# Optimization experiments

Measured on AMD Instinct MI355X. Metric: run time of the kernel, lower is better.

## Reference

```python
import jax, jax.numpy as jnp
import numpy as np

B, D, H, HD, L = 2, 768, 16, 48, 3
N_IMG, N_PAST, T_DEC = 1024, 16, 20

def _ln(x, g, b, eps=1e-5):
    m = jnp.mean(x, axis=-1, keepdims=True)
    v = jnp.mean(jnp.square(x - m), axis=-1, keepdims=True)
    return (x - m) * jax.lax.rsqrt(v + eps) * g + b

def _encoder(x, ln1_g, ln1_b, qkv_W, qkv_b, out_W, out_b, ln2_g, ln2_b, ff1_W, ff1_b, ff2_W, ff2_b):
    Bs, S, _ = x.shape
    keep = jnp.tril(jnp.ones((S, S), dtype=bool))  # causal: True = attend
    neg = jnp.asarray(jnp.finfo(x.dtype).min, x.dtype)
    scale = 1.0 / np.sqrt(HD)
    for l in range(L):  # pre-norm TransformerEncoderLayer, activation=relu (torch default)
        h = _ln(x, ln1_g[l], ln1_b[l])
        q, k, v = jnp.split(h @ qkv_W[l] + qkv_b[l], 3, axis=-1)
        q = q.reshape(Bs, S, H, HD); k = k.reshape(Bs, S, H, HD); v = v.reshape(Bs, S, H, HD)
        scores = jnp.einsum('bqhd,bkhd->bhqk', q, k) * scale
        attn = jax.nn.softmax(jnp.where(keep, scores, neg), axis=-1)
        ctx = jnp.einsum('bhqk,bkhd->bqhd', attn, v).reshape(Bs, S, H * HD)
        x = x + ctx @ out_W[l] + out_b[l]
        h = _ln(x, ln2_g[l], ln2_b[l])
        x = x + jax.nn.relu(h @ ff1_W[l] + ff1_b[l]) @ ff2_W[l] + ff2_b[l]
    return x

def setup_inputs():
    key = jax.random.key(0)
    ks = jax.random.split(key, 16)
    rn = lambda i, shp, s=0.02: jax.random.normal(ks[i], shp, jnp.float32) * s
    return {
        'feats': jax.random.normal(ks[0], (B, D, N_IMG), jnp.float32),
        'past': jax.random.normal(ks[1], (B, N_PAST, 6), jnp.float32),
        'intent': jax.random.randint(ks[2], (B,), 0, 3),
        'img_pos_enc': rn(3, (1, N_IMG, D)),
        'time_embeds': rn(4, (36, D)),
        'intent_embeds': rn(5, (3, D)),
        'past_W': rn(6, (6, D)), 'past_b': jnp.zeros((D,), jnp.float32),
        'pos_W': rn(7, (2, D)), 'pos_b': jnp.zeros((D,), jnp.float32),
        'ln1_g': jnp.ones((L, D), jnp.float32), 'ln1_b': jnp.zeros((L, D), jnp.float32),
        'qkv_W': rn(8, (L, D, 3 * D)), 'qkv_b': jnp.zeros((L, 3 * D), jnp.float32),
        'out_W': rn(9, (L, D, D)), 'out_b': jnp.zeros((L, D), jnp.float32),
        'ln2_g': jnp.ones((L, D), jnp.float32), 'ln2_b': jnp.zeros((L, D), jnp.float32),
        'ff1_W': rn(10, (L, D, 4 * D)), 'ff1_b': jnp.zeros((L, 4 * D), jnp.float32),
        'ff2_W': rn(11, (L, 4 * D, D)), 'ff2_b': jnp.zeros((L, D), jnp.float32),
        'dec1_W': rn(12, (D, D)), 'dec1_b': jnp.zeros((D,), jnp.float32),
        'dec2_W': rn(13, (D, 2)), 'dec2_b': jnp.zeros((2,), jnp.float32),
    }

def reference(feats, past, intent, img_pos_enc, time_embeds, intent_embeds,
              past_W, past_b, pos_W, pos_b,
              ln1_g, ln1_b, qkv_W, qkv_b, out_W, out_b, ln2_g, ln2_b,
              ff1_W, ff1_b, ff2_W, ff2_b, dec1_W, dec1_b, dec2_W, dec2_b):
    # context: 1024 image tokens + 1 intent token + 16 past tokens
    img_tokens = jnp.transpose(feats, (0, 2, 1)) + img_pos_enc          # [B, 1024, D]
    intent_idx = jnp.clip(intent - 1, 0, 2)
    intent_tok = intent_embeds[intent_idx][:, None, :]                  # [B, 1, D]
    past_toks = past @ past_W + past_b + time_embeds[:N_PAST]           # [B, 16, D]
    seq = jnp.concatenate([img_tokens, intent_tok, past_toks], axis=1)  # [B, 1041, D]
    enc = lambda s: _encoder(s, ln1_g, ln1_b, qkv_W, qkv_b, out_W, out_b,
                             ln2_g, ln2_b, ff1_W, ff1_b, ff2_W, ff2_b)
    preds = []
    for t in range(T_DEC):  # AR decode: full recompute each step, no KV cache (as in source)
        out = enc(seq)
        h = out[:, -1:, :]
        p = jax.nn.gelu(h @ dec1_W + dec1_b, approximate=False) @ dec2_W + dec2_b  # [B,1,2]
        preds.append(p)
        nxt = p @ pos_W + pos_b + time_embeds[N_PAST + t]
        seq = jnp.concatenate([seq, nxt], axis=1)
    return jnp.concatenate(preds, axis=1)  # [B, 20, 2]
```

## Files before the change

### kernel.cpp

```cpp
#include <hip/hip_runtime.h>
#include <math.h>

#define BB 2
#define DD 768
#define HH 16
#define HDIM 48
#define LL 3
#define NIMG 1024
#define NPAST 16
#define TDEC 20
#define SEQ0 1041
#define SPAD 1064
#define MM (BB*SEQ0)
#define SCALE_QK 0.14433756729740643f
#define KVL_C ((size_t)BB*HH*SPAD*HDIM)

typedef __attribute__((ext_vector_type(4))) float f32x4;
typedef __attribute__((ext_vector_type(8))) short bf16x8;

__device__ __forceinline__ short f2bf(float x) {
  unsigned u = __float_as_uint(x);
  unsigned r = (u + 0x7FFFu + ((u >> 16) & 1u)) >> 16;
  return (short)r;
}
__device__ __forceinline__ float bf2f(short h) {
  return __uint_as_float(((unsigned)(unsigned short)h) << 16);
}

__device__ __forceinline__ float block_sum256(float v, float* red) {
#pragma unroll
  for (int off = 32; off; off >>= 1) v += __shfl_down(v, off);
  __syncthreads();
  if ((threadIdx.x & 63) == 0) red[threadIdx.x >> 6] = v;
  __syncthreads();
  return red[0] + red[1] + red[2] + red[3];
}

__global__ __launch_bounds__(256) void build_img_kernel(
    const float* __restrict__ feats, const float* __restrict__ pe, float* __restrict__ x)
{
  __shared__ float T[64][65];
  int b = blockIdx.y;
  int s0 = blockIdx.x * 64;
  int tid = threadIdx.x;
  int r = tid >> 2;
  int c0 = (tid & 3) << 4;
  for (int d0 = 0; d0 < 768; d0 += 64) {
    const float* fp = feats + ((size_t)b*768 + d0 + r)*1024 + s0 + c0;
#pragma unroll
    for (int i = 0; i < 16; ++i) T[r][c0 + i] = fp[i];
    __syncthreads();
    float* xp = x + ((size_t)(b*SEQ0 + s0 + r))*768 + d0 + c0;
    const float* pp = pe + (size_t)(s0 + r)*768 + d0 + c0;
#pragma unroll
    for (int i = 0; i < 16; ++i) xp[i] = T[c0 + i][r] + pp[i];
    __syncthreads();
  }
}

__global__ __launch_bounds__(256) void build_misc_kernel(
    const float* __restrict__ past, const int* __restrict__ intent,
    const float* __restrict__ int_emb, const float* __restrict__ past_W,
    const float* __restrict__ past_b, const float* __restrict__ te,
    float* __restrict__ x)
{
  int b = blockIdx.y;
  int i = blockIdx.x;
  int tid = threadIdx.x;
  if (i == 0) {
    int idx = intent[b] - 1;
    idx = max(0, min(2, idx));
    for (int d = tid; d < 768; d += 256)
      x[((size_t)(b*SEQ0 + 1024))*768 + d] = int_emb[idx*768 + d];
  } else {
    int pi = i - 1;
    float p0 = past[(b*NPAST + pi)*6 + 0], p1 = past[(b*NPAST + pi)*6 + 1];
    float p2 = past[(b*NPAST + pi)*6 + 2], p3 = past[(b*NPAST + pi)*6 + 3];
    float p4 = past[(b*NPAST + pi)*6 + 4], p5 = past[(b*NPAST + pi)*6 + 5];
    for (int d = tid; d < 768; d += 256) {
      float s = past_b[d] + te[(size_t)pi*768 + d];
      s += p0*past_W[0*768 + d] + p1*past_W[1*768 + d] + p2*past_W[2*768 + d];
      s += p3*past_W[3*768 + d] + p4*past_W[4*768 + d] + p5*past_W[5*768 + d];
      x[((size_t)(b*SEQ0 + 1025 + pi))*768 + d] = s;
    }
  }
}

__global__ __launch_bounds__(256) void ln_bf_kernel(
    const float* __restrict__ x, const float* __restrict__ g,
    const float* __restrict__ bta, short* __restrict__ hh, short* __restrict__ hl)
{
  __shared__ float red[4];
  size_t row = blockIdx.x;
  const float* xr = x + row*768;
  int tid = threadIdx.x;
  float v0 = xr[tid], v1 = xr[tid+256], v2 = xr[tid+512];
  float m = block_sum256(v0+v1+v2, red) * (1.f/768.f);
  float d0 = v0-m, d1 = v1-m, d2 = v2-m;
  float var = block_sum256(d0*d0 + d1*d1 + d2*d2, red) * (1.f/768.f);
  float inv = rsqrtf(var + 1e-5f);
  float o0 = d0*inv*g[tid]     + bta[tid];
  float o1 = d1*inv*g[tid+256] + bta[tid+256];
  float o2 = d2*inv*g[tid+512] + bta[tid+512];
  short h0 = f2bf(o0), h1 = f2bf(o1), h2 = f2bf(o2);
  size_t base = row*768;
  hh[base+tid]     = h0; hl[base+tid]     = f2bf(o0 - bf2f(h0));
  hh[base+tid+256] = h1; hl[base+tid+256] = f2bf(o1 - bf2f(h1));
  hh[base+tid+512] = h2; hl[base+tid+512] = f2bf(o2 - bf2f(h2));
}

__global__ __launch_bounds__(256) void wconv_kernel(
    const float* __restrict__ W, short* __restrict__ th, short* __restrict__ tl,
    int K, int N)
{
  __shared__ float T[64][68];
  int n0 = blockIdx.x * 64, k0 = blockIdx.y * 64;
  int t = threadIdx.x;
  int r = t >> 2, c0 = (t & 3) * 16;
  const float* src = W + (size_t)(k0 + r)*N + n0 + c0;
#pragma unroll
  for (int j = 0; j < 4; ++j) {
    f32x4 v = *(const f32x4*)(src + 4*j);
    T[r][c0 + 4*j + 0] = v.x; T[r][c0 + 4*j + 1] = v.y;
    T[r][c0 + 4*j + 2] = v.z; T[r][c0 + 4*j + 3] = v.w;
  }
  __syncthreads();
  bf16x8 h0, h1, l0, l1;
#pragma unroll
  for (int i = 0; i < 8; ++i) {
    float x = T[c0 + i][r];
    short hh = f2bf(x);
    h0[i] = hh; l0[i] = f2bf(x - bf2f(hh));
    float y = T[c0 + 8 + i][r];
    short hy = f2bf(y);
    h1[i] = hy; l1[i] = f2bf(y - bf2f(hy));
  }
  size_t dst = (size_t)(n0 + r)*K + k0 + c0;
  *(bf16x8*)(th + dst) = h0;
  *(bf16x8*)(th + dst + 8) = h1;
  *(bf16x8*)(tl + dst) = l0;
  *(bf16x8*)(tl + dst + 8) = l1;
}

__global__ __launch_bounds__(256) void gemm_bf_kernel(
    const short* __restrict__ Ah, const short* __restrict__ Al,
    const short* __restrict__ Wh, const short* __restrict__ Wl,
    const float* __restrict__ bias, float* __restrict__ C,
    short* __restrict__ Ch, short* __restrict__ Cl,
    int M, int N, int K, int mode,
    float* __restrict__ kc, float* __restrict__ vc)
{
  __shared__ short As[2][128][40];
  __shared__ short Bs[2][128][40];
  int tid = threadIdx.x;
  int n0 = blockIdx.x * 128, m0 = blockIdx.y * 128;
  int wid = tid >> 6, l = tid & 63;
  int wm = wid >> 1, wn = wid & 1;
  int fr = l & 15, fk = (l >> 4) * 8;
  f32x4 acc[4][4] = {};
  int arow = tid >> 1, akh = (tid & 1) * 16;
  bool aval = (m0 + arow) < M;
  size_t abase = (size_t)(m0 + arow)*K + akh;

  for (int k0 = 0; k0 < K; k0 += 32) {
    if (aval) {
      size_t src = abase + k0;
      *(bf16x8*)&As[0][arow][akh]     = *(const bf16x8*)(Ah + src);
      *(bf16x8*)&As[0][arow][akh + 8] = *(const bf16x8*)(Ah + src + 8);
      *(bf16x8*)&As[1][arow][akh]     = *(const bf16x8*)(Al + src);
      *(bf16x8*)&As[1][arow][akh + 8] = *(const bf16x8*)(Al + src + 8);
    } else {
      bf16x8 z = {};
      *(bf16x8*)&As[0][arow][akh] = z; *(bf16x8*)&As[0][arow][akh + 8] = z;
      *(bf16x8*)&As[1][arow][akh] = z; *(bf16x8*)&As[1][arow][akh + 8] = z;
    }
#pragma unroll
    for (int cc = 0; cc < 2; ++cc) {
      int c = tid + cc*256;
      int row = c >> 2, woff = (c & 3) * 8;
      size_t src = (size_t)(n0 + row)*K + k0 + woff;
      *(bf16x8*)&Bs[0][row][woff] = *(const bf16x8*)(Wh + src);
      *(bf16x8*)&Bs[1][row][woff] = *(const bf16x8*)(Wl + src);
    }
    __syncthreads();
    bf16x8 af[4][2], bfv[4][2];
#pragma unroll
    for (int i = 0; i < 4; ++i) {
#pragma unroll
      for (int p = 0; p < 2; ++p) {
        af[i][p]  = *(const bf16x8*)&As[p][wm*64 + i*16 + fr][fk];
        bfv[i][p] = *(const bf16x8*)&Bs[p][wn*64 + i*16 + fr][fk];
      }
    }
#pragma unroll
    for (int im = 0; im < 4; ++im) {
#pragma unroll
      for (int in = 0; in < 4; ++in) {
        acc[im][in] = __builtin_amdgcn_mfma_f32_16x16x32_bf16(af[im][0], bfv[in][0], acc[im][in], 0, 0, 0);
        acc[im][in] = __builtin_amdgcn_mfma_f32_16x16x32_bf16(af[im][0], bfv[in][1], acc[im][in], 0, 0, 0);
        acc[im][in] = __builtin_amdgcn_mfma_f32_16x16x32_bf16(af[im][1], bfv[in][0], acc[im][in], 0, 0, 0);
      }
    }
    __syncthreads();
  }
#pragma unroll
  for (int in = 0; in < 4; ++in) {
    int n = n0 + wn*64 + in*16 + (l & 15);
    float bv = bias[n];
#pragma unroll
    for (int im = 0; im < 4; ++im) {
      f32x4 v = acc[im][in];
#pragma unroll
      for (int r = 0; r < 4; ++r) {
        int m = m0 + wm*64 + im*16 + (l >> 4)*4 + r;
        if (m < M) {
          float x = v[r] + bv;
          size_t off = (size_t)m*N + n;
          if (mode == 1) {
            x = fmaxf(x, 0.f);
            short hh = f2bf(x);
            Ch[off] = hh;
            Cl[off] = f2bf(x - bf2f(hh));
          } else if (mode == 2) {
            C[off] += x;
          } else {
            C[off] = x;
            if (mode == 3 && n >= 768) {
              int b = m / SEQ0, s = m - b*SEQ0;
              int j = n - 768;
              if (j < 768)
                kc[((size_t)(b*16 + j/48)*SPAD + s)*48 + (j % 48)] = x;
              else {
                j -= 768;
                vc[((size_t)(b*16 + j/48)*SPAD + s)*48 + (j % 48)] = x;
              }
            }
          }
        }
      }
    }
  }
}

__global__ __launch_bounds__(256) void attn_prefill_kernel(
    const float* __restrict__ qkv, const float* __restrict__ Kc,
    const float* __restrict__ Vc, short* __restrict__ ctxh, short* __restrict__ ctxl,
    int S, int spad)
{
  __shared__ float Qs[32][49];
  __shared__ float Ks[64][49];
  __shared__ float Vs[64][49];
  __shared__ float Ps[32][65];
  __shared__ float mrow[32], lrow[32], resc[32];
  int tid = threadIdx.x;
  int qt = blockIdx.x, h = blockIdx.y, b = blockIdx.z;
  int q0 = qt * 32;
  for (int i = tid; i < 32*48; i += 256) {
    int r = i / 48, d = i - r*48;
    int s = q0 + r;
    Qs[r][d] = (s < S) ? qkv[((size_t)(b*S + s))*2304 + h*48 + d] * SCALE_QK : 0.f;
  }
  if (tid < 32) { mrow[tid] = -INFINITY; lrow[tid] = 0.f; }
  float acc[2][3] = {};
  int pr0 = (tid >> 4) << 1;
  int pc  = tid & 15;
  int sr  = tid & 31;
  int skg = tid >> 5;
  int q_last = min(q0 + 31, S - 1);
  const float* Kb = Kc + (size_t)(b*16 + h)*spad*48;
  const float* Vb = Vc + (size_t)(b*16 + h)*spad*48;
  __syncthreads();
  float qreg[48];
#pragma unroll
  for (int d = 0; d < 48; ++d) qreg[d] = Qs[sr][d];
  for (int k0 = 0; k0 <= q_last; k0 += 64) {
    int kn = min(64, q_last - k0 + 1);
    for (int i = tid; i < 64*48; i += 256) {
      int r = i / 48, d = i - r*48;
      bool ok = r < kn;
      Ks[r][d] = ok ? Kb[(size_t)(k0 + r)*48 + d] : 0.f;
      Vs[r][d] = ok ? Vb[(size_t)(k0 + r)*48 + d] : 0.f;
    }
    __syncthreads();
    {
      int qg = q0 + sr;
#pragma unroll
      for (int jj = 0; jj < 8; ++jj) {
        int k = skg*8 + jj;
        float s = 0.f;
#pragma unroll
        for (int d = 0; d < 48; ++d) s += qreg[d] * Ks[k][d];
        int kg = k0 + k;
        bool valid = (qg < S) && (k < kn) && (kg <= qg);
        Ps[sr][k] = valid ? s : -INFINITY;
      }
    }
    __syncthreads();
    {
      int r = tid >> 3;
      int c0 = (tid & 7) * 8;
      float mold = mrow[r];
      float mx = mold;
      float pv[8];
#pragma unroll
      for (int j = 0; j < 8; ++j) { pv[j] = Ps[r][c0 + j]; mx = fmaxf(mx, pv[j]); }
#pragma unroll
      for (int m = 1; m < 8; m <<= 1) mx = fmaxf(mx, __shfl_xor(mx, m));
      float psum = 0.f;
      if (mx > -INFINITY) {
#pragma unroll
        for (int j = 0; j < 8; ++j) {
          float p = __expf(pv[j] - mx);
          Ps[r][c0 + j] = p;
          psum += p;
        }
      } else {
#pragma unroll
        for (int j = 0; j < 8; ++j) Ps[r][c0 + j] = 0.f;
      }
#pragma unroll
      for (int m = 1; m < 8; m <<= 1) psum += __shfl_xor(psum, m);
      if ((tid & 7) == 0) {
        if (mx > -INFINITY) {
          float rs = (mold > -INFINITY) ? __expf(mold - mx) : 0.f;
          lrow[r] = lrow[r]*rs + psum;
          mrow[r] = mx;
          resc[r] = rs;
        } else {
          resc[r] = 1.f;
        }
      }
    }
    __syncthreads();
#pragma unroll
    for (int rr = 0; rr < 2; ++rr) {
      int r = pr0 + rr;
      float f = resc[r];
      float a0 = acc[rr][0]*f, a1 = acc[rr][1]*f, a2 = acc[rr][2]*f;
#pragma unroll 16
      for (int k = 0; k < 64; ++k) {
        float p = Ps[r][k];
        a0 += p * Vs[k][pc*3+0];
        a1 += p * Vs[k][pc*3+1];
        a2 += p * Vs[k][pc*3+2];
      }
      acc[rr][0] = a0; acc[rr][1] = a1; acc[rr][2] = a2;
    }
    __syncthreads();
  }
#pragma unroll
  for (int rr = 0; rr < 2; ++rr) {
    int r = pr0 + rr, s = q0 + r;
    if (s < S) {
      float invl = 1.f / lrow[r];
      size_t off = ((size_t)(b*S + s))*768 + h*48 + pc*3;
#pragma unroll
      for (int j = 0; j < 3; ++j) {
        float val = acc[rr][j]*invl;
        short hh = f2bf(val);
        ctxh[off + j] = hh;
        ctxl[off + j] = f2bf(val - bf2f(hh));
      }
    }
  }
}

struct DecParams {
  const float *qkv_W, *qkv_b, *out_W, *out_b;
  const float *ln1_g, *ln1_b, *ln2_g, *ln2_b;
  const float *ff1_W, *ff1_b, *ff2_W, *ff2_b;
  const float *dec1_W, *dec1_b, *dec2_W, *dec2_b;
  const float *pos_W, *pos_b, *time_e;
  const float *xlast;
  float *Kc, *Vc;
  float *x_tok, *x_in_buf, *x_mid_buf;
  float *qkv_part, *out_part, *ff1_part, *ff2_part, *dec1_part;
  float *attn_m, *attn_l, *attn_o;
  float *outp;
};

__global__ __launch_bounds__(256) void k_qkvA(DecParams P, int l) {
  int p = blockIdx.x;
  __shared__ float xin[2][768];
  __shared__ float hn[2][768];
  __shared__ float part[4][2][64];
  __shared__ float red[4];
  int tid = threadIdx.x;
  if (l == 0) {
    for (int i = tid; i < 1536; i += 256) ((float*)xin)[i] = P.x_tok[i];
  } else {
    for (int i = tid; i < 1536; i += 256) {
      float v = P.x_mid_buf[i];
#pragma unroll
      for (int s = 0; s < 21; ++s) v += P.ff2_part[s*1536 + i];
      ((float*)xin)[i] = v;
    }
  }
  __syncthreads();
  if (p == 0) {
    for (int i = tid; i < 1536; i += 256) P.x_in_buf[i] = ((float*)xin)[i];
  }
  const float* g  = P.ln1_g + l*768;
  const float* be = P.ln1_b + l*768;
#pragma unroll
  for (int b = 0; b < 2; ++b) {
    float v0 = xin[b][tid], v1 = xin[b][tid+256], v2 = xin[b][tid+512];
    float m = block_sum256(v0+v1+v2, red) * (1.f/768.f);
    float d0=v0-m, d1=v1-m, d2=v2-m;
    float var = block_sum256(d0*d0+d1*d1+d2*d2, red) * (1.f/768.f);
    float inv = rsqrtf(var + 1e-5f);
    hn[b][tid]     = d0*inv*g[tid]     + be[tid];
    hn[b][tid+256] = d1*inv*g[tid+256] + be[tid+256];
    hn[b][tid+512] = d2*inv*g[tid+512] + be[tid+512];
  }
  __syncthreads();
  int nt = p % 36, ks = p / 36;
  int k0 = (ks*768)/7, k1 = ((ks+1)*768)/7;
  int w = tid >> 6, lane = tid & 63;
  int kw0 = k0 + ((k1-k0)*w)/4, kw1 = k0 + ((k1-k0)*(w+1))/4;
  int n = nt*64 + lane;
  const float* wp = P.qkv_W + (size_t)l*768*2304 + n;
  float a0 = 0.f, a1 = 0.f;
#pragma unroll 4
  for (int k = kw0; k < kw1; ++k) {
    float w_ = wp[(size_t)k*2304];
    a0 += hn[0][k]*w_; a1 += hn[1][k]*w_;
  }
  part[w][0][lane] = a0; part[w][1][lane] = a1;
  __syncthreads();
  if (tid < 128) {
    int b = tid>>6, ln = tid&63;
    float s = part[0][b][ln]+part[1][b][ln]+part[2][b][ln]+part[3][b][ln];
    P.qkv_part[ks*4608 + b*2304 + nt*64 + ln] = s;
  }
}

__global__ __launch_bounds__(256) void k_attn(DecParams P, int l, int pos) {
  __shared__ float qs[48], ksn[48], vsn[48];
  __shared__ float redm[4], reds[4];
  __shared__ float aw[4][48];
  int p = blockIdx.x;
  int b = p >> 7, h = (p >> 3) & 15, s = p & 7;
  int tid = threadIdx.x;
  const float* qb = P.qkv_b + l*2304;
  if (tid < 48) {
    float q  = qb[h*48+tid];
    float kk = qb[768 + h*48+tid];
    float vv = qb[1536 + h*48+tid];
#pragma unroll
    for (int ss = 0; ss < 7; ++ss) {
      const float* pp = P.qkv_part + ss*4608 + b*2304;
      q  += pp[h*48+tid];
      kk += pp[768 + h*48+tid];
      vv += pp[1536 + h*48+tid];
    }
    if (s == 7) {
      size_t coff = (size_t)l*KVL_C + ((size_t)(b*16+h)*SPAD + pos)*48 + tid;
      P.Kc[coff] = kk;
      P.Vc[coff] = vv;
    }
    qs[tid] = q * SCALE_QK; ksn[tid] = kk; vsn[tid] = vv;
  }
  __syncthreads();
  int CH = (pos + 7) >> 3;
  int r0 = s*CH, r1 = min(r0 + CH, pos);
  int nold = r1 - r0;
  bool is_new = (s == 7) && (tid == nold);
  bool active = (tid < nold) || is_new;
  const float* Kb = P.Kc + (size_t)l*KVL_C + (size_t)(b*16+h)*SPAD*48;
  const float* Vb = P.Vc + (size_t)l*KVL_C + (size_t)(b*16+h)*SPAD*48;
  float sc = -INFINITY;
  if (tid < nold) {
    const float4* kr = (const float4*)(Kb + (size_t)(r0+tid)*48);
    float ssum = 0.f;
#pragma unroll
    for (int i = 0; i < 12; ++i) {
      float4 kv = kr[i];
      ssum += qs[4*i]*kv.x + qs[4*i+1]*kv.y + qs[4*i+2]*kv.z + qs[4*i+3]*kv.w;
    }
    sc = ssum;
  } else if (is_new) {
    float ssum = 0.f;
#pragma unroll
    for (int d = 0; d < 48; ++d) ssum += qs[d]*ksn[d];
    sc = ssum;
  }
  float mx = sc;
#pragma unroll
  for (int o2 = 32; o2; o2 >>= 1) mx = fmaxf(mx, __shfl_down(mx, o2));
  if ((tid & 63) == 0) redm[tid >> 6] = mx;
  __syncthreads();
  float M = fmaxf(fmaxf(redm[0], redm[1]), fmaxf(redm[2], redm[3]));
  float pr = active ? __expf(sc - M) : 0.f;
  float lsum = block_sum256(pr, reds);
  float4 a[12];
  if (tid < nold) {
    const float4* vr = (const float4*)(Vb + (size_t)(r0+tid)*48);
#pragma unroll
    for (int i = 0; i < 12; ++i) {
      float4 vv = vr[i];
      a[i].x = pr*vv.x; a[i].y = pr*vv.y; a[i].z = pr*vv.z; a[i].w = pr*vv.w;
    }
  } else if (is_new) {
#pragma unroll
    for (int i = 0; i < 12; ++i) {
      a[i].x = pr*vsn[4*i]; a[i].y = pr*vsn[4*i+1];
      a[i].z = pr*vsn[4*i+2]; a[i].w = pr*vsn[4*i+3];
    }
  } else {
#pragma unroll
    for (int i = 0; i < 12; ++i) a[i] = make_float4(0.f,0.f,0.f,0.f);
  }
#pragma unroll
  for (int i = 0; i < 12; ++i) {
    float x0=a[i].x, x1=a[i].y, x2=a[i].z, x3=a[i].w;
#pragma unroll
    for (int o2 = 32; o2; o2 >>= 1) {
      x0 += __shfl_down(x0, o2); x1 += __shfl_down(x1, o2);
      x2 += __shfl_down(x2, o2); x3 += __shfl_down(x3, o2);
    }
    if ((tid & 63) == 0) {
      int w = tid >> 6;
      aw[w][4*i] = x0; aw[w][4*i+1] = x1; aw[w][4*i+2] = x2; aw[w][4*i+3] = x3;
    }
  }
  __syncthreads();
  int idx = (b*16 + h)*8 + s;
  if (tid == 0) { P.attn_m[idx] = M; P.attn_l[idx] = lsum; }
  if (tid < 48) P.attn_o[idx*48 + tid] = aw[0][tid]+aw[1][tid]+aw[2][tid]+aw[3][tid];
}

__global__ __launch_bounds__(256) void k_out(DecParams P, int l) {
  int p = blockIdx.x;
  __shared__ float ctx_s[2][96];
  __shared__ float opart[4][2][64][2];
  int nt = p / 8, ks = p % 8;
  int k0 = ks * 96;
  int tid = threadIdx.x;
  if (tid < 192) {
    int b = tid / 96, dl = tid % 96;
    int d = k0 + dl;
    int h = d / 48, dd = d % 48;
    int base = (b*16 + h)*8;
    float M = -INFINITY;
#pragma unroll
    for (int s2 = 0; s2 < 8; ++s2) M = fmaxf(M, P.attn_m[base+s2]);
    float L = 0.f, o = 0.f;
#pragma unroll
    for (int s2 = 0; s2 < 8; ++s2) {
      float e = __expf(P.attn_m[base+s2] - M);
      L += P.attn_l[base+s2]*e;
      o += P.attn_o[(base+s2)*48 + dd]*e;
    }
    ctx_s[b][dl] = o / L;
  }
  __syncthreads();
  int w = tid >> 6, lane = tid & 63;
  int n0 = nt * 128;
  const float* W = P.out_W + (size_t)l*768*768;
  float a00=0.f, a01=0.f, a10=0.f, a11=0.f;
#pragma unroll 4
  for (int j = w*24; j < w*24 + 24; ++j) {
    int kk = k0 + j;
    float2 wv = *(const float2*)&W[(size_t)kk*768 + n0 + lane*2];
    float c0 = ctx_s[0][j], c1 = ctx_s[1][j];
    a00 += c0*wv.x; a01 += c0*wv.y;
    a10 += c1*wv.x; a11 += c1*wv.y;
  }
  opart[w][0][lane][0] = a00; opart[w][0][lane][1] = a01;
  opart[w][1][lane][0] = a10; opart[w][1][lane][1] = a11;
  __syncthreads();
  {
    int b = tid >> 7, idx = tid & 127;
    int l2 = idx >> 1, c = idx & 1;
    float v = opart[0][b][l2][c] + opart[1][b][l2][c]
            + opart[2][b][l2][c] + opart[3][b][l2][c];
    P.out_part[ks*1536 + b*768 + n0 + idx] = v;
  }
}

__global__ __launch_bounds__(256) void k_ff1A(DecParams P, int l) {
  int p = blockIdx.x;
  __shared__ float xm[2][768];
  __shared__ float hn[2][768];
  __shared__ float part[4][2][64];
  __shared__ float red[4];
  int tid = threadIdx.x;
  const float* ob = P.out_b + l*768;
  for (int i = tid; i < 1536; i += 256) {
    int b = i / 768, d = i - b*768;
    float v = P.x_in_buf[i] + ob[d];
#pragma unroll
    for (int s = 0; s < 8; ++s) v += P.out_part[s*1536 + i];
    xm[b][d] = v;
  }
  __syncthreads();
  if (p == 0) {
    for (int i = tid; i < 1536; i += 256) P.x_mid_buf[i] = ((float*)xm)[i];
  }
  const float* g  = P.ln2_g + l*768;
  const float* be = P.ln2_b + l*768;
#pragma unroll
  for (int b = 0; b < 2; ++b) {
    float v0 = xm[b][tid], v1 = xm[b][tid+256], v2 = xm[b][tid+512];
    float m = block_sum256(v0+v1+v2, red) * (1.f/768.f);
    float d0=v0-m, d1=v1-m, d2=v2-m;
    float var = block_sum256(d0*d0+d1*d1+d2*d2, red) * (1.f/768.f);
    float inv = rsqrtf(var + 1e-5f);
    hn[b][tid]     = d0*inv*g[tid]     + be[tid];
    hn[b][tid+256] = d1*inv*g[tid+256] + be[tid+256];
    hn[b][tid+512] = d2*inv*g[tid+512] + be[tid+512];
  }
  __syncthreads();
  int nt = p % 48, ks = p / 48;
  int k0 = (ks*768)/5, k1 = ((ks+1)*768)/5;
  int w = tid >> 6, lane = tid & 63;
  int kw0 = k0 + ((k1-k0)*w)/4, kw1 = k0 + ((k1-k0)*(w+1))/4;
  int n = nt*64 + lane;
  const float* wp = P.ff1_W + (size_t)l*768*3072 + n;
  float a0 = 0.f, a1 = 0.f;
#pragma unroll 4
  for (int k = kw0; k < kw1; ++k) {
    float w_ = wp[(size_t)k*3072];
    a0 += hn[0][k]*w_; a1 += hn[1][k]*w_;
  }
  part[w][0][lane] = a0; part[w][1][lane] = a1;
  __syncthreads();
  if (tid < 128) {
    int b = tid>>6, ln = tid&63;
    float s = part[0][b][ln]+part[1][b][ln]+part[2][b][ln]+part[3][b][ln];
    P.ff1_part[ks*6144 + b*3072 + nt*64 + ln] = s;
  }
}

__global__ __launch_bounds__(256) void k_ff2A(DecParams P, int l) {
  int p = blockIdx.x;
  __shared__ float hseg[2][148];
  __shared__ float part[4][2][64];
  int tid = threadIdx.x;
  int nt = p % 12, ks = p / 12;
  int k0 = (ks*3072)/21, k1 = ((ks+1)*3072)/21;
  int kn = k1 - k0;
  const float* fb = P.ff1_b + l*3072;
  for (int i = tid; i < 2*kn; i += 256) {
    int b = i / kn, j = i - b*kn;
    float v = fb[k0+j];
#pragma unroll
    for (int s = 0; s < 5; ++s) v += P.ff1_part[s*6144 + b*3072 + k0 + j];
    hseg[b][j] = fmaxf(v, 0.f);
  }
  __syncthreads();
  int w = tid >> 6, lane = tid & 63;
  int jw0 = (kn*w)/4, jw1 = (kn*(w+1))/4;
  int n = nt*64 + lane;
  const float* wp = P.ff2_W + (size_t)l*3072*768 + n;
  float a0 = 0.f, a1 = 0.f;
#pragma unroll 4
  for (int j = jw0; j < jw1; ++j) {
    float w_ = wp[(size_t)(k0+j)*768];
    a0 += hseg[0][j]*w_; a1 += hseg[1][j]*w_;
  }
  part[w][0][lane] = a0; part[w][1][lane] = a1;
  __syncthreads();
  if (tid < 128) {
    int b = tid>>6, ln = tid&63;
    P.ff2_part[ks*1536 + b*768 + nt*64 + ln] =
        part[0][b][ln]+part[1][b][ln]+part[2][b][ln]+part[3][b][ln];
  }
}

__global__ __launch_bounds__(256) void k_dec1A(DecParams P, int t) {
  int p = blockIdx.x;
  __shared__ float hseg[2][40];
  __shared__ float part[4][2][64];
  int tid = threadIdx.x;
  int nt = p % 12, ks = p / 12;
  int k0 = (ks*768)/21, k1 = ((ks+1)*768)/21;
  int kn = k1 - k0;
  for (int i = tid; i < 2*kn; i += 256) {
    int b = i / kn, j = i - b*kn;
    float v;
    if (t == 0) {
      v = P.xlast[(size_t)b*SEQ0*768 + k0 + j];
    } else {
      v = P.x_mid_buf[b*768 + k0 + j];
#pragma unroll
      for (int s = 0; s < 21; ++s) v += P.ff2_part[s*1536 + b*768 + k0 + j];
    }
    hseg[b][j] = v;
  }
  __syncthreads();
  int w = tid >> 6, lane = tid & 63;
  int jw0 = (kn*w)/4, jw1 = (kn*(w+1))/4;
  int n = nt*64 + lane;
  const float* wp = P.dec1_W + n;
  float a0 = 0.f, a1 = 0.f;
#pragma unroll 4
  for (int j = jw0; j < jw1; ++j) {
    float w_ = wp[(size_t)(k0+j)*768];
    a0 += hseg[0][j]*w_; a1 += hseg[1][j]*w_;
  }
  part[w][0][lane] = a0; part[w][1][lane] = a1;
  __syncthreads();
  if (tid < 128) {
    int b = tid>>6, ln = tid&63;
    P.dec1_part[ks*1536 + b*768 + nt*64 + ln] =
        part[0][b][ln]+part[1][b][ln]+part[2][b][ln]+part[3][b][ln];
  }
}

__global__ __launch_bounds__(256) void k_head2(DecParams P, int t, int write_next) {
  __shared__ float hd[2][768];
  __shared__ float ps[2][2];
  int tid = threadIdx.x;
  for (int i = tid; i < 1536; i += 256) {
    int b = i / 768, d = i - b*768;
    float v = P.dec1_b[d];
#pragma unroll
    for (int s = 0; s < 21; ++s) v += P.dec1_part[s*1536 + i];
    hd[b][d] = 0.5f*v*(1.f + erff(v*0.70710678118654752f));
  }
  __syncthreads();
  int w = tid >> 6, lane = tid & 63;
  int b = w >> 1, j = w & 1;
  float partial = 0.f;
  for (int k = lane; k < 768; k += 64) partial += hd[b][k] * P.dec2_W[k*2 + j];
#pragma unroll
  for (int off = 32; off; off >>= 1) partial += __shfl_down(partial, off);
  if (lane == 0) {
    float v = partial + P.dec2_b[j];
    ps[b][j] = v;
    P.outp[(b*TDEC + t)*2 + j] = v;
  }
  __syncthreads();
  if (write_next) {
    for (int i = tid; i < 1536; i += 256) {
      int b2 = i / 768, d = i - b2*768;
      P.x_tok[i] = ps[b2][0]*P.pos_W[d] + ps[b2][1]*P.pos_W[768 + d]
                 + P.pos_b[d] + P.time_e[(size_t)(NPAST + t)*768 + d];
    }
  }
}

extern "C" void kernel_launch(void* const* d_in, const int* in_sizes, int n_in,
                              void* d_out, int out_size, void* d_ws, size_t ws_size,
                              hipStream_t stream) {
  (void)in_sizes; (void)n_in; (void)out_size; (void)ws_size;
  const float* feats   = (const float*)d_in[0];
  const float* past    = (const float*)d_in[1];
  const int*   intent  = (const int*)d_in[2];
  const float* img_pos = (const float*)d_in[3];
  const float* time_e  = (const float*)d_in[4];
  const float* int_emb = (const float*)d_in[5];
  const float* past_W  = (const float*)d_in[6];
  const float* past_b  = (const float*)d_in[7];
  const float* pos_W   = (const float*)d_in[8];
  const float* pos_b   = (const float*)d_in[9];
  const float* ln1_g   = (const float*)d_in[10];
  const float* ln1_b   = (const float*)d_in[11];
  const float* qkv_W   = (const float*)d_in[12];
  const float* qkv_b   = (const float*)d_in[13];
  const float* out_W   = (const float*)d_in[14];
  const float* out_b   = (const float*)d_in[15];
  const float* ln2_g   = (const float*)d_in[16];
  const float* ln2_b   = (const float*)d_in[17];
  const float* ff1_W   = (const float*)d_in[18];
  const float* ff1_b   = (const float*)d_in[19];
  const float* ff2_W   = (const float*)d_in[20];
  const float* ff2_b   = (const float*)d_in[21];
  const float* dec1_W  = (const float*)d_in[22];
  const float* dec1_b  = (const float*)d_in[23];
  const float* dec2_W  = (const float*)d_in[24];
  const float* dec2_b  = (const float*)d_in[25];
  float* outp = (float*)d_out;

  float* ws = (float*)d_ws;
  size_t off = 0;
  float* xbuf = ws + off;   off += (size_t)MM*DD;
  short* hh = (short*)(ws + off); off += (size_t)MM*DD/2;
  short* hl = (short*)(ws + off); off += (size_t)MM*DD/2;
  float* bigbuf = ws + off; off += (size_t)MM*3072;
  short* bigh = (short*)bigbuf;
  short* bigl = bigh + (size_t)MM*3072;
  float* Kc = ws + off;     off += (size_t)LL*BB*HH*SPAD*HDIM;
  float* Vc = ws + off;     off += (size_t)LL*BB*HH*SPAD*HDIM;
  float* x_tok = ws + off;    off += BB*DD;
  float* x_in_buf = ws + off; off += BB*DD;
  float* x_mid_buf = ws + off; off += BB*DD;
  float* qkv_part = ws + off;  off += 7*2*2304;
  float* out_part = ws + off;  off += 8*2*768;
  float* ff1_part = ws + off;  off += 5*2*3072;
  float* ff2_part = ws + off;  off += 21*2*768;
  float* dec1_part = ws + off; off += 21*2*768;
  float* attn_m = ws + off;    off += 2*16*8;
  float* attn_l = ws + off;    off += 2*16*8;
  float* attn_o = ws + off;    off += 2*16*8*48;
  short* wt_h = (short*)(ws + off); off += (size_t)768*3072/2;
  short* wt_l = (short*)(ws + off); off += (size_t)768*3072/2;

  const size_t KVL = (size_t)BB*HH*SPAD*HDIM;

  build_img_kernel<<<dim3(NIMG/64, BB), 256, 0, stream>>>(feats, img_pos, xbuf);
  build_misc_kernel<<<dim3(17, BB), 256, 0, stream>>>(past, intent, int_emb, past_W, past_b, time_e, xbuf);

  const int mtiles = (MM + 127) / 128;
  for (int l = 0; l < LL; ++l) {
    float* kcl = Kc + (size_t)l*KVL;
    float* vcl = Vc + (size_t)l*KVL;

    ln_bf_kernel<<<MM, 256, 0, stream>>>(xbuf, ln1_g + l*DD, ln1_b + l*DD, hh, hl);
    wconv_kernel<<<dim3(2304/64, 768/64), 256, 0, stream>>>(
        qkv_W + (size_t)l*DD*2304, wt_h, wt_l, DD, 2304);
    gemm_bf_kernel<<<dim3(2304/128, mtiles), 256, 0, stream>>>(
        hh, hl, wt_h, wt_l, qkv_b + l*2304, bigbuf, nullptr, nullptr,
        MM, 2304, DD, 3, kcl, vcl);

    attn_prefill_kernel<<<dim3((SEQ0 + 31)/32, HH, BB), 256, 0, stream>>>(
        bigbuf, kcl, vcl, hh, hl, SEQ0, SPAD);

    wconv_kernel<<<dim3(768/64, 768/64), 256, 0, stream>>>(
        out_W + (size_t)l*DD*DD, wt_h, wt_l, DD, 768);
    gemm_bf_kernel<<<dim3(768/128, mtiles), 256, 0, stream>>>(
        hh, hl, wt_h, wt_l, out_b + l*DD, xbuf, nullptr, nullptr,
        MM, 768, DD, 2, nullptr, nullptr);

    ln_bf_kernel<<<MM, 256, 0, stream>>>(xbuf, ln2_g + l*DD, ln2_b + l*DD, hh, hl);
    wconv_kernel<<<dim3(3072/64, 768/64), 256, 0, stream>>>(
        ff1_W + (size_t)l*DD*3072, wt_h, wt_l, DD, 3072);
    gemm_bf_kernel<<<dim3(3072/128, mtiles), 256, 0, stream>>>(
        hh, hl, wt_h, wt_l, ff1_b + l*3072, nullptr, bigh, bigl,
        MM, 3072, DD, 1, nullptr, nullptr);

    wconv_kernel<<<dim3(768/64, 3072/64), 256, 0, stream>>>(
        ff2_W + (size_t)l*3072*DD, wt_h, wt_l, 3072, 768);
    gemm_bf_kernel<<<dim3(768/128, mtiles), 256, 0, stream>>>(
        bigh, bigl, wt_h, wt_l, ff2_b + l*DD, xbuf, nullptr, nullptr,
        MM, 768, 3072, 2, nullptr, nullptr);
  }

  DecParams P;
  P.qkv_W = qkv_W; P.qkv_b = qkv_b; P.out_W = out_W; P.out_b = out_b;
  P.ln1_g = ln1_g; P.ln1_b = ln1_b; P.ln2_g = ln2_g; P.ln2_b = ln2_b;
  P.ff1_W = ff1_W; P.ff1_b = ff1_b; P.ff2_W = ff2_W; P.ff2_b = ff2_b;
  P.dec1_W = dec1_W; P.dec1_b = dec1_b; P.dec2_W = dec2_W; P.dec2_b = dec2_b;
  P.pos_W = pos_W; P.pos_b = pos_b; P.time_e = time_e;
  P.xlast = xbuf + (size_t)(SEQ0 - 1)*DD;
  P.Kc = Kc; P.Vc = Vc;
  P.x_tok = x_tok; P.x_in_buf = x_in_buf; P.x_mid_buf = x_mid_buf;
  P.qkv_part = qkv_part; P.out_part = out_part; P.ff1_part = ff1_part;
  P.ff2_part = ff2_part; P.dec1_part = dec1_part;
  P.attn_m = attn_m; P.attn_l = attn_l; P.attn_o = attn_o;
  P.outp = outp;

  k_dec1A<<<252, 256, 0, stream>>>(P, 0);
  k_head2<<<1, 256, 0, stream>>>(P, 0, 1);
  for (int t = 1; t < TDEC; ++t) {
    int pos = SEQ0 + t - 1;
    for (int l = 0; l < LL; ++l) {
      k_qkvA<<<252, 256, 0, stream>>>(P, l);
      k_attn<<<256, 256, 0, stream>>>(P, l, pos);
      k_out<<<48, 256, 0, stream>>>(P, l);
      k_ff1A<<<240, 256, 0, stream>>>(P, l);
      k_ff2A<<<252, 256, 0, stream>>>(P, l);
    }
    k_dec1A<<<252, 256, 0, stream>>>(P, t);
    k_head2<<<1, 256, 0, stream>>>(P, t, (t < TDEC - 1) ? 1 : 0);
  }
}
```

Baseline: 4.831 ms.

## Fuse autoregressive decode phases into one persistent kernel with grid barriers

```diff
diff --git a/kernel.cpp b/kernel.cpp
--- a/kernel.cpp
+++ b/kernel.cpp
@@ -12,6 +12,7 @@
 #define SEQ0 1041
 #define SPAD 1064
 #define MM (BB*SEQ0)
+#define GDEC 256
 #define SCALE_QK 0.14433756729740643f
 #define KVL_C ((size_t)BB*HH*SPAD*HDIM)
 
@@ -34,6 +35,39 @@
   if ((threadIdx.x & 63) == 0) red[threadIdx.x >> 6] = v;
   __syncthreads();
   return red[0] + red[1] + red[2] + red[3];
+}
+
+__device__ __forceinline__ void gbar(unsigned* slots, unsigned* gen,
+                                     unsigned bar_no, unsigned nb) {
+  __syncthreads();
+  int tid = threadIdx.x;
+  if (blockIdx.x == 0) {
+    if (tid > 0 && tid < (int)nb) {
+      while (__hip_atomic_load(&slots[(size_t)tid*16], __ATOMIC_RELAXED,
+                               __HIP_MEMORY_SCOPE_AGENT) < bar_no)
+        __builtin_amdgcn_s_sleep(1);
+    }
+    __syncthreads();
+    if (tid == 0) {
+      __builtin_amdgcn_fence(__ATOMIC_ACQUIRE, "agent");
+      __hip_atomic_store(gen, bar_no, __ATOMIC_RELEASE, __HIP_MEMORY_SCOPE_AGENT);
+    }
+  } else {
+    if (tid == 0) {
+      __hip_atomic_store(&slots[(size_t)blockIdx.x*16], bar_no,
+                         __ATOMIC_RELEASE, __HIP_MEMORY_SCOPE_AGENT);
+      while (__hip_atomic_load(gen, __ATOMIC_RELAXED,
+                               __HIP_MEMORY_SCOPE_AGENT) < bar_no)
+        __builtin_amdgcn_s_sleep(1);
+      __builtin_amdgcn_fence(__ATOMIC_ACQUIRE, "agent");
+    }
+  }
+  __syncthreads();
+}
+
+__global__ void bar_init_kernel(unsigned* bar) {
+  int tid = threadIdx.x;
+  for (int i = tid; i < 256*16 + 16; i += 256) bar[i] = 0u;
 }
 
 __global__ __launch_bounds__(256) void build_img_kernel(
@@ -377,10 +411,12 @@
   float *qkv_part, *out_part, *ff1_part, *ff2_part, *dec1_part;
   float *attn_m, *attn_l, *attn_o;
   float *outp;
+  unsigned *slots, *gen;
 };
 
-__global__ __launch_bounds__(256) void k_qkvA(DecParams P, int l) {
+__device__ void ph_qkvA(const DecParams& P, int l) {
   int p = blockIdx.x;
+  if (p >= 252) return;
   __shared__ float xin[2][768];
   __shared__ float hn[2][768];
   __shared__ float part[4][2][64];
@@ -435,7 +471,7 @@
   }
 }
 
-__global__ __launch_bounds__(256) void k_attn(DecParams P, int l, int pos) {
+__device__ void ph_attn(const DecParams& P, int l, int pos) {
   __shared__ float qs[48], ksn[48], vsn[48];
   __shared__ float redm[4], reds[4];
   __shared__ float aw[4][48];
@@ -530,8 +566,9 @@
   if (tid < 48) P.attn_o[idx*48 + tid] = aw[0][tid]+aw[1][tid]+aw[2][tid]+aw[3][tid];
 }
 
-__global__ __launch_bounds__(256) void k_out(DecParams P, int l) {
+__device__ void ph_out(const DecParams& P, int l) {
   int p = blockIdx.x;
+  if (p >= 48) return;
   __shared__ float ctx_s[2][96];
   __shared__ float opart[4][2][64][2];
   int nt = p / 8, ks = p % 8;
@@ -579,8 +616,9 @@
   }
 }
 
-__global__ __launch_bounds__(256) void k_ff1A(DecParams P, int l) {
+__device__ void ph_ff1A(const DecParams& P, int l) {
   int p = blockIdx.x;
+  if (p >= 240) return;
   __shared__ float xm[2][768];
   __shared__ float hn[2][768];
   __shared__ float part[4][2][64];
@@ -633,8 +671,9 @@
   }
 }
 
-__global__ __launch_bounds__(256) void k_ff2A(DecParams P, int l) {
+__device__ void ph_ff2A(const DecParams& P, int l) {
   int p = blockIdx.x;
+  if (p >= 252) return;
   __shared__ float hseg[2][148];
   __shared__ float part[4][2][64];
   int tid = threadIdx.x;
@@ -669,8 +708,9 @@
   }
 }
 
-__global__ __launch_bounds__(256) void k_dec1A(DecParams P, int t) {
+__device__ void ph_dec1A(const DecParams& P, int t) {
   int p = blockIdx.x;
+  if (p >= 252) return;
   __shared__ float hseg[2][40];
   __shared__ float part[4][2][64];
   int tid = threadIdx.x;
@@ -709,7 +749,8 @@
   }
 }
 
-__global__ __launch_bounds__(256) void k_head2(DecParams P, int t, int write_next) {
+__device__ void ph_head2(const DecParams& P, int t, int write_next) {
+  if (blockIdx.x != 0) return;
   __shared__ float hd[2][768];
   __shared__ float ps[2][2];
   int tid = threadIdx.x;
@@ -739,6 +780,35 @@
       P.x_tok[i] = ps[b2][0]*P.pos_W[d] + ps[b2][1]*P.pos_W[768 + d]
                  + P.pos_b[d] + P.time_e[(size_t)(NPAST + t)*768 + d];
     }
+  }
+}
+
+__global__ __launch_bounds__(256, 1) void decode_persistent_kernel(DecParams P)
+{
+  const unsigned nb = gridDim.x;
+  unsigned bno = 0;
+  ph_dec1A(P, 0);
+  ++bno; gbar(P.slots, P.gen, bno, nb);
+  ph_head2(P, 0, 1);
+  ++bno; gbar(P.slots, P.gen, bno, nb);
+  for (int t = 1; t < TDEC; ++t) {
+    int pos = SEQ0 + t - 1;
+    for (int l = 0; l < LL; ++l) {
+      ph_qkvA(P, l);
+      ++bno; gbar(P.slots, P.gen, bno, nb);
+      ph_attn(P, l, pos);
+      ++bno; gbar(P.slots, P.gen, bno, nb);
+      ph_out(P, l);
+      ++bno; gbar(P.slots, P.gen, bno, nb);
+      ph_ff1A(P, l);
+      ++bno; gbar(P.slots, P.gen, bno, nb);
+      ph_ff2A(P, l);
+      ++bno; gbar(P.slots, P.gen, bno, nb);
+    }
+    ph_dec1A(P, t);
+    ++bno; gbar(P.slots, P.gen, bno, nb);
+    ph_head2(P, t, (t < TDEC - 1) ? 1 : 0);
+    ++bno; gbar(P.slots, P.gen, bno, nb);
   }
 }
 
@@ -797,6 +867,7 @@
   float* attn_o = ws + off;    off += 2*16*8*48;
   short* wt_h = (short*)(ws + off); off += (size_t)768*3072/2;
   short* wt_l = (short*)(ws + off); off += (size_t)768*3072/2;
+  unsigned* bar = (unsigned*)(ws + off); off += 256*16 + 16;
 
   const size_t KVL = (size_t)BB*HH*SPAD*HDIM;
 
@@ -838,6 +909,7 @@
         MM, 768, 3072, 2, nullptr, nullptr);
   }
 
+  bar_init_kernel<<<1, 256, 0, stream>>>(bar);
   DecParams P;
   P.qkv_W = qkv_W; P.qkv_b = qkv_b; P.out_W = out_W; P.out_b = out_b;
   P.ln1_g = ln1_g; P.ln1_b = ln1_b; P.ln2_g = ln2_g; P.ln2_b = ln2_b;
@@ -851,19 +923,6 @@
   P.ff2_part = ff2_part; P.dec1_part = dec1_part;
   P.attn_m = attn_m; P.attn_l = attn_l; P.attn_o = attn_o;
   P.outp = outp;
-
-  k_dec1A<<<252, 256, 0, stream>>>(P, 0);
-  k_head2<<<1, 256, 0, stream>>>(P, 0, 1);
-  for (int t = 1; t < TDEC; ++t) {
-    int pos = SEQ0 + t - 1;
-    for (int l = 0; l < LL; ++l) {
-      k_qkvA<<<252, 256, 0, stream>>>(P, l);
-      k_attn<<<256, 256, 0, stream>>>(P, l, pos);
-      k_out<<<48, 256, 0, stream>>>(P, l);
-      k_ff1A<<<240, 256, 0, stream>>>(P, l);
-      k_ff2A<<<252, 256, 0, stream>>>(P, l);
-    }
-    k_dec1A<<<252, 256, 0, stream>>>(P, t);
-    k_head2<<<1, 256, 0, stream>>>(P, t, (t < TDEC - 1) ? 1 : 0);
-  }
-}
+  P.slots = bar; P.gen = bar + 256*16;
+  decode_persistent_kernel<<<GDEC, 256, 0, stream>>>(P);
+}
```

After: 8.948 ms. 85.2% more time.
